# Kernel optimization log

Hardware: AMD Instinct MI355X
Metric: run time of the kernel (lower is better)

Reference implementation:

```python
import jax, jax.numpy as jnp
import numpy as np

B, N = 1, 512
C_S, C_Z, C_H, H, PQ, PV = 384, 128, 16, 12, 4, 8
INF, EPS = 1e5, 1e-8
HW_INIT = 0.541324854612918  # softplus^{-1}(1), ipa_point_weights_init_


def _rotary(t, rot_dim, theta=10000.0):
    # lucidrains interleaved rotary over residue axis (axis 1); rotates first rot_dim channels
    n = t.shape[1]
    inv_freq = 1.0 / (theta ** (jnp.arange(0, rot_dim, 2, dtype=jnp.float32) / rot_dim))
    freqs = jnp.arange(n, dtype=jnp.float32)[:, None] * inv_freq  # [N, rot_dim//2]
    cos = jnp.cos(freqs)[None, :, None, :].astype(t.dtype)
    sin = jnp.sin(freqs)[None, :, None, :].astype(t.dtype)
    tr, tp = t[..., :rot_dim], t[..., rot_dim:]
    x1, x2 = tr[..., 0::2], tr[..., 1::2]
    tr = jnp.stack([x1 * cos - x2 * sin, x1 * sin + x2 * cos], axis=-1).reshape(tr.shape)
    return jnp.concatenate([tr, tp], axis=-1)


def _ipa(s, z, rot, trans, mask, Wq, bq, Wkv, bkv, Wqp, bqp, Wkvp, bkvp, Wb, bb,
         head_weights, Whid, bhid, Wpair, bpair, Wpts, bpts, Wpn, bpn):
    Bx, Nx = s.shape[0], s.shape[1]
    q = (s @ Wq + bq).reshape(Bx, Nx, H, C_H)
    kv = (s @ Wkv + bkv).reshape(Bx, Nx, H, 2 * C_H)
    k, v = kv[..., :C_H], kv[..., C_H:]

    def make_pts(x, npts):
        # channel layout: [x-block, y-block, z-block] -> [B,N,H*npts,3], then rigid apply R@p+t
        x = jnp.stack(jnp.split(x, 3, axis=-1), axis=-1)
        x = jnp.einsum('bnij,bnpj->bnpi', rot, x) + trans[:, :, None, :]
        return x.reshape(Bx, Nx, H, npts, 3)

    q_pts = make_pts(s @ Wqp + bqp, PQ)
    kv_pts = make_pts(s @ Wkvp + bkvp, PQ + PV)
    k_pts, v_pts = kv_pts[..., :PQ, :], kv_pts[..., PQ:, :]

    q = _rotary(q, C_H // 2)
    k = _rotary(k, C_H // 2)

    a = jnp.einsum('bihc,bjhc->bhij', q, k) * np.sqrt(1.0 / (3 * C_H))
    a = a + np.sqrt(1.0 / 3.0) * (jnp.einsum('bijc,ch->bhij', z, Wb) + bb[None, :, None, None])
    d2 = jnp.sum((q_pts[:, :, None] - k_pts[:, None]) ** 2, axis=-1)  # [B,Ni,Nj,H,PQ]
    hw = jax.nn.softplus(head_weights) * np.sqrt(1.0 / (3 * (PQ * 9.0 / 2)))
    a = a + jnp.transpose(-0.5 * jnp.sum(d2 * hw[None, None, None, :, None], axis=-1), (0, 3, 1, 2))
    sq_mask = INF * (mask[:, :, None] * mask[:, None, :] - 1.0)
    a = jax.nn.softmax(a + sq_mask[:, None], axis=-1)  # [B,H,N,N]

    o = jnp.einsum('bhij,bjhc->bihc', a, v).reshape(Bx, Nx, H * C_H)
    o_pt = jnp.einsum('bhij,bjhpx->bihpx', a, v_pts)  # [B,N,H,PV,3]
    o_pt = jnp.einsum('bnji,bnhpj->bnhpi', rot, o_pt - trans[:, :, None, None, :])  # invert_apply
    o_pt_norm = jnp.sqrt(jnp.sum(o_pt ** 2, axis=-1) + EPS).reshape(Bx, Nx, H * PV)
    o_pt = o_pt.reshape(Bx, Nx, H * PV, 3)
    pts_feat = jnp.concatenate([o_pt[..., 0], o_pt[..., 1], o_pt[..., 2]], axis=-1)
    o_pair = jnp.einsum('bhij,bijc->bihc', a, z).reshape(Bx, Nx, H * C_Z)

    s_out = ((o @ Whid + bhid) + (o_pair @ Wpair + bpair)
             + (pts_feat @ Wpts + bpts) + (o_pt_norm @ Wpn + bpn))
    return s_out, a


def setup_inputs() -> dict:
    key = jax.random.key(0)
    ks = jax.random.split(key, 16)
    f = lambda i, shape: jax.random.normal(ks[i], shape, dtype=jnp.float32)
    sc = 0.02
    rot, _ = jnp.linalg.qr(f(2, (B, N, 3, 3)))
    return {
        's': f(0, (B, N, C_S)),
        'z': f(1, (B, N, N, C_Z)),
        'rot': rot,
        'trans': f(3, (B, N, 3)),
        'mask': jnp.ones((B, N), jnp.float32),
        'Wq': f(4, (C_S, H * C_H)) * sc, 'bq': jnp.zeros((H * C_H,), jnp.float32),
        'Wkv': f(5, (C_S, 2 * H * C_H)) * sc, 'bkv': jnp.zeros((2 * H * C_H,), jnp.float32),
        'Wqp': f(6, (C_S, H * PQ * 3)) * sc, 'bqp': jnp.zeros((H * PQ * 3,), jnp.float32),
        'Wkvp': f(7, (C_S, H * (PQ + PV) * 3)) * sc, 'bkvp': jnp.zeros((H * (PQ + PV) * 3,), jnp.float32),
        'Wb': f(8, (C_Z, H)) * sc, 'bb': jnp.zeros((H,), jnp.float32),
        'head_weights': jnp.full((H,), HW_INIT, jnp.float32),
        'Whid': f(9, (H * C_H, C_S)) * sc, 'bhid': jnp.zeros((C_S,), jnp.float32),
        'Wpair': f(10, (H * C_Z, C_S)) * sc, 'bpair': jnp.zeros((C_S,), jnp.float32),
        'Wpts': f(11, (H * PV * 3, C_S)) * sc, 'bpts': jnp.zeros((C_S,), jnp.float32),
        'Wpn': f(12, (H * PV, C_S)) * sc, 'bpn': jnp.zeros((C_S,), jnp.float32),
    }


def reference(s, z, rot, trans, mask, Wq, bq, Wkv, bkv, Wqp, bqp, Wkvp, bkvp, Wb, bb,
              head_weights, Whid, bhid, Wpair, bpair, Wpts, bpts, Wpn, bpn):
    return _ipa(s, z, rot, trans, mask, Wq, bq, Wkv, bkv, Wqp, bqp, Wkvp, bkvp, Wb, bb,
                head_weights, Whid, bhid, Wpair, bpair, Wpts, bpts, Wpn, bpn)
```

## Files before the change

kernel.cpp:

```cpp
#include <hip/hip_runtime.h>
#include <hip/hip_bf16.h>
#include <cmath>

#define N 512
#define C_S 384
#define C_Z 128
#define C_H 16
#define H 12
#define PQ 4
#define PV 8

#define NJC 4
#define JCHUNK (N / NJC)
#define NPART 2016
#define NFEAT 2112
#define NRAW 1152
#define KSPLIT 11
#define KCHUNK 192

#define WS_Q    0
#define WS_K    (WS_Q + N*H*C_H)
#define WS_V    (WS_K + N*H*C_H)
#define WS_QP   (WS_V + N*H*C_H)
#define WS_KP   (WS_QP + N*H*PQ*3)
#define WS_VP   (WS_KP + N*H*PQ*3)
#define WS_PART (WS_VP + N*H*PV*3)
#define WS_FEAT (WS_PART + N*NJC*NPART)
#define WS_RAW  WS_PART
#define WS_KT   (WS_PART + 1200000)
#define WS_KPT  (WS_KT + 98304)
#define WS_WBT  (WS_KPT + 73728)
#define WS_FOUT WS_PART

__global__ __launch_bounds__(256) void k_gemm_proj(
    const float* __restrict__ s,
    const float* __restrict__ Wq,  const float* __restrict__ bq,
    const float* __restrict__ Wkv, const float* __restrict__ bkv,
    const float* __restrict__ Wqp, const float* __restrict__ bqp,
    const float* __restrict__ Wkvp,const float* __restrict__ bkvp,
    float* __restrict__ raw_out)
{
    const int m0 = blockIdx.x * 64;
    const int c0 = blockIdx.y * 64;
    const int t  = threadIdx.x;
    const int tc = t & 15;
    const int tm = t >> 4;

    __shared__ float st[64 * 33];
    __shared__ float wt[32 * 64];

    float acc[4][4];
#pragma unroll
    for (int u = 0; u < 4; ++u) {
        int col = c0 + tc*4 + u;
        const float* b; int cb;
        if (col < 192)      { b = bq;   cb = 0; }
        else if (col < 576) { b = bkv;  cb = 192; }
        else if (col < 720) { b = bqp;  cb = 576; }
        else                { b = bkvp; cb = 720; }
        float bv = b[col - cb];
#pragma unroll
        for (int r = 0; r < 4; ++r) acc[r][u] = bv;
    }

    for (int k0 = 0; k0 < C_S; k0 += 32) {
        __syncthreads();
        for (int e = t; e < 512; e += 256) {
            int row = e >> 3, kq = e & 7;
            float4 v = *(const float4*)&s[(size_t)(m0 + row)*C_S + k0 + kq*4];
            st[row*33 + kq*4 + 0] = v.x;
            st[row*33 + kq*4 + 1] = v.y;
            st[row*33 + kq*4 + 2] = v.z;
            st[row*33 + kq*4 + 3] = v.w;
        }
        for (int e = t; e < 512; e += 256) {
            int kk = e >> 4, c4 = e & 15;
            int col = c0 + c4*4;
            const float* W; int ncol, cb;
            if (col < 192)      { W = Wq;   ncol = 192; cb = 0; }
            else if (col < 576) { W = Wkv;  ncol = 384; cb = 192; }
            else if (col < 720) { W = Wqp;  ncol = 144; cb = 576; }
            else                { W = Wkvp; ncol = 432; cb = 720; }
            float4 v = *(const float4*)&W[(size_t)(k0 + kk)*ncol + (col - cb)];
            *(float4*)&wt[kk*64 + c4*4] = v;
        }
        __syncthreads();

#pragma unroll 8
        for (int kk = 0; kk < 32; ++kk) {
            float4 w = *(const float4*)&wt[kk*64 + tc*4];
            float sv[4];
#pragma unroll
            for (int r = 0; r < 4; ++r) sv[r] = st[(tm*4 + r)*33 + kk];
#pragma unroll
            for (int r = 0; r < 4; ++r) {
                acc[r][0] += sv[r] * w.x;
                acc[r][1] += sv[r] * w.y;
                acc[r][2] += sv[r] * w.z;
                acc[r][3] += sv[r] * w.w;
            }
        }
    }

#pragma unroll
    for (int r = 0; r < 4; ++r) {
        float4 o = make_float4(acc[r][0], acc[r][1], acc[r][2], acc[r][3]);
        *(float4*)&raw_out[(size_t)(m0 + tm*4 + r)*NRAW + c0 + tc*4] = o;
    }
}

__global__ __launch_bounds__(256) void k_post(
    const float* __restrict__ raw_in, const float* __restrict__ rot,
    const float* __restrict__ trans, const float* __restrict__ Wb,
    float* __restrict__ ws)
{
    const int n = blockIdx.x;
    const int t = threadIdx.x;
    __shared__ float raw[NRAW];

    for (int idx = t; idx < NRAW; idx += 256) raw[idx] = raw_in[(size_t)n*NRAW + idx];
    __syncthreads();

    if (n == 0) {
        for (int idx = t; idx < H*C_Z; idx += 256) {
            int h = idx >> 7, c = idx & 127;
            ws[WS_WBT + h*128 + c] = Wb[c*H + h];
        }
    }

    float R[9], T[3];
#pragma unroll
    for (int u = 0; u < 9; ++u) R[u] = rot[n*9 + u];
#pragma unroll
    for (int u = 0; u < 3; ++u) T[u] = trans[n*3 + u];

    float* q    = ws + WS_Q;
    float* v    = ws + WS_V;
    float* qp   = ws + WS_QP;
    float* vp   = ws + WS_VP;
    float* kT4  = ws + WS_KT;
    float* kpT4 = ws + WS_KPT;

    for (int idx = t; idx < 1152; idx += 256) {
        if (idx < 192) {
            int h = idx >> 4, c = idx & 15;
            float val;
            if (c < 8) {
                int f = c >> 1;
                float x1 = raw[h*16 + 2*f];
                float x2 = raw[h*16 + 2*f + 1];
                float ang = (float)n * powf(10000.0f, -(float)(2*f) / 8.0f);
                float cs = cosf(ang), sn = sinf(ang);
                val = (c & 1) ? (x1*sn + x2*cs) : (x1*cs - x2*sn);
            } else {
                val = raw[h*16 + c];
            }
            q[n*192 + idx] = val;
        } else if (idx < 384) {
            int o = idx - 192, h = o >> 4, c = o & 15;
            float val;
            if (c < 8) {
                int f = c >> 1;
                float x1 = raw[192 + h*32 + 2*f];
                float x2 = raw[192 + h*32 + 2*f + 1];
                float ang = (float)n * powf(10000.0f, -(float)(2*f) / 8.0f);
                float cs = cosf(ang), sn = sinf(ang);
                val = (c & 1) ? (x1*sn + x2*cs) : (x1*cs - x2*sn);
            } else {
                val = raw[192 + h*32 + c];
            }
            kT4[((size_t)(o >> 2)*N + n)*4 + (o & 3)] = val;
        } else if (idx < 576) {
            int o = idx - 384, h = o >> 4, c = o & 15;
            v[n*192 + o] = raw[192 + h*32 + 16 + c];
        } else if (idx < 720) {
            int o = idx - 576;
            int hp = o / 3, ic = o - hp*3;
            float acc = T[ic];
#pragma unroll
            for (int j = 0; j < 3; ++j) acc += R[ic*3 + j] * raw[576 + j*48 + hp];
            qp[n*144 + o] = acc;
        } else {
            int o = idx - 720;
            int hp = o / 3, ic = o - hp*3;
            int h = hp / 12, p = hp - h*12;
            float acc = T[ic];
#pragma unroll
            for (int j = 0; j < 3; ++j) acc += R[ic*3 + j] * raw[720 + j*144 + hp];
            if (p < PQ) {
                int e = h*12 + p*3 + ic;
                kpT4[((size_t)(e >> 2)*N + n)*4 + (e & 3)] = acc;
            } else {
                vp[n*(H*PV*3) + (h*PV + (p - PQ))*3 + ic] = acc;
            }
        }
    }
}

__global__ __launch_bounds__(256) void k_logits(
    const float* __restrict__ ws, const float* __restrict__ z,
    const float* __restrict__ bb,
    const float* __restrict__ hwts, const float* __restrict__ mask,
    float* __restrict__ a_out)
{
    const int i  = blockIdx.x;
    const int j0 = blockIdx.y * 64;
    const int t  = threadIdx.x;
    const int j  = t & 63;
    const int jg = j0 + j;
    const int h0 = __builtin_amdgcn_readfirstlane(3 * (t >> 6));

    __shared__ float zt[64*132];

    float4 ra0, ra1, ra2, ra3, rb0, rb1, rb2, rb3;
    {
        const float* zbase = z + (((size_t)i*N) + j0)*C_Z;
        int e0 = t,       r0_ = e0 >> 4, c0_ = e0 & 15;
        int e1 = t + 256, r1_ = e1 >> 4, c1_ = e1 & 15;
        int e2 = t + 512, r2_ = e2 >> 4, c2_ = e2 & 15;
        int e3 = t + 768, r3_ = e3 >> 4, c3_ = e3 & 15;
        ra0 = *(const float4*)&zbase[(size_t)r0_*C_Z + c0_*4];
        ra1 = *(const float4*)&zbase[(size_t)r1_*C_Z + c1_*4];
        ra2 = *(const float4*)&zbase[(size_t)r2_*C_Z + c2_*4];
        ra3 = *(const float4*)&zbase[(size_t)r3_*C_Z + c3_*4];
        rb0 = *(const float4*)&zbase[(size_t)r0_*C_Z + 64 + c0_*4];
        rb1 = *(const float4*)&zbase[(size_t)r1_*C_Z + 64 + c1_*4];
        rb2 = *(const float4*)&zbase[(size_t)r2_*C_Z + 64 + c2_*4];
        rb3 = *(const float4*)&zbase[(size_t)r3_*C_Z + 64 + c3_*4];
    }

    const float* q    = ws + WS_Q  + (size_t)i*192;
    const float* qp   = ws + WS_QP + (size_t)i*144;
    const float* kT4  = ws + WS_KT;
    const float* kpT4 = ws + WS_KPT;

    const float c1 = sqrtf(1.0f / 48.0f);
    const float c2 = sqrtf(1.0f / 3.0f);
    const float mterm = 100000.0f * (mask[i] * mask[jg] - 1.0f);

    float qkd[3];
#pragma unroll
    for (int u = 0; u < 3; ++u) {
        const int h = h0 + u;
        float qk = 0.0f;
#pragma unroll
        for (int cq = 0; cq < 4; ++cq) {
            float4 kv = *(const float4*)&kT4[((size_t)(h*4 + cq)*N + jg)*4];
            qk += q[h*16 + cq*4 + 0]*kv.x + q[h*16 + cq*4 + 1]*kv.y
                + q[h*16 + cq*4 + 2]*kv.z + q[h*16 + cq*4 + 3]*kv.w;
        }
        float d2s = 0.0f;
#pragma unroll
        for (int eq = 0; eq < 3; ++eq) {
            float4 pv = *(const float4*)&kpT4[((size_t)(h*3 + eq)*N + jg)*4];
            float d;
            d = qp[h*12 + eq*4 + 0] - pv.x; d2s += d*d;
            d = qp[h*12 + eq*4 + 1] - pv.y; d2s += d*d;
            d = qp[h*12 + eq*4 + 2] - pv.z; d2s += d*d;
            d = qp[h*12 + eq*4 + 3] - pv.w; d2s += d*d;
        }
        float hw = log1pf(expf(hwts[h])) * sqrtf(1.0f / 54.0f);
        qkd[u] = c1*qk - 0.5f*hw*d2s + mterm + c2*bb[h];
    }

    {
        int e0 = t,       r0_ = e0 >> 4, c0_ = e0 & 15;
        int e1 = t + 256, r1_ = e1 >> 4, c1_ = e1 & 15;
        int e2 = t + 512, r2_ = e2 >> 4, c2_ = e2 & 15;
        int e3 = t + 768, r3_ = e3 >> 4, c3_ = e3 & 15;
        *(float4*)&zt[r0_*132 + c0_*4] = ra0;
        *(float4*)&zt[r1_*132 + c1_*4] = ra1;
        *(float4*)&zt[r2_*132 + c2_*4] = ra2;
        *(float4*)&zt[r3_*132 + c3_*4] = ra3;
    }
    __syncthreads();

    const float* w0 = ws + WS_WBT + (size_t)h0*128;
    float acc[3] = {0.0f, 0.0f, 0.0f};
#pragma unroll
    for (int c4 = 0; c4 < 16; ++c4) {
        float4 zv = *(const float4*)&zt[j*132 + c4*4];
        float4 b0 = *(const float4*)&w0[c4*4];
        float4 b1 = *(const float4*)&w0[128 + c4*4];
        float4 b2 = *(const float4*)&w0[256 + c4*4];
        acc[0] += zv.x*b0.x + zv.y*b0.y + zv.z*b0.z + zv.w*b0.w;
        acc[1] += zv.x*b1.x + zv.y*b1.y + zv.z*b1.z + zv.w*b1.w;
        acc[2] += zv.x*b2.x + zv.y*b2.y + zv.z*b2.z + zv.w*b2.w;
    }
    __syncthreads();

    {
        int e0 = t,       r0_ = e0 >> 4, c0_ = e0 & 15;
        int e1 = t + 256, r1_ = e1 >> 4, c1_ = e1 & 15;
        int e2 = t + 512, r2_ = e2 >> 4, c2_ = e2 & 15;
        int e3 = t + 768, r3_ = e3 >> 4, c3_ = e3 & 15;
        *(float4*)&zt[r0_*132 + 64 + c0_*4] = rb0;
        *(float4*)&zt[r1_*132 + 64 + c1_*4] = rb1;
        *(float4*)&zt[r2_*132 + 64 + c2_*4] = rb2;
        *(float4*)&zt[r3_*132 + 64 + c3_*4] = rb3;
    }
    __syncthreads();

#pragma unroll
    for (int c4 = 16; c4 < 32; ++c4) {
        float4 zv = *(const float4*)&zt[j*132 + c4*4];
        float4 b0 = *(const float4*)&w0[c4*4];
        float4 b1 = *(const float4*)&w0[128 + c4*4];
        float4 b2 = *(const float4*)&w0[256 + c4*4];
        acc[0] += zv.x*b0.x + zv.y*b0.y + zv.z*b0.z + zv.w*b0.w;
        acc[1] += zv.x*b1.x + zv.y*b1.y + zv.z*b1.z + zv.w*b1.w;
        acc[2] += zv.x*b2.x + zv.y*b2.y + zv.z*b2.z + zv.w*b2.w;
    }

#pragma unroll
    for (int u = 0; u < 3; ++u)
        a_out[((size_t)(h0 + u)*N + i)*N + jg] = qkd[u] + c2*acc[u];
}

__global__ __launch_bounds__(256) void k_softmax(float* __restrict__ a)
{
    const int row  = blockIdx.x*4 + (threadIdx.x >> 6);
    const int lane = threadIdx.x & 63;
    float* r = a + (size_t)row * N;

    float v[8];
    float m = -1e30f;
#pragma unroll
    for (int u = 0; u < 8; ++u) { v[u] = r[lane + 64*u]; m = fmaxf(m, v[u]); }
#pragma unroll
    for (int off = 32; off; off >>= 1) m = fmaxf(m, __shfl_xor(m, off));
    float ssum = 0.0f;
#pragma unroll
    for (int u = 0; u < 8; ++u) { v[u] = expf(v[u] - m); ssum += v[u]; }
#pragma unroll
    for (int off = 32; off; off >>= 1) ssum += __shfl_xor(ssum, off);
    float inv = 1.0f / ssum;
#pragma unroll
    for (int u = 0; u < 8; ++u) r[lane + 64*u] = v[u] * inv;
}

__global__ __launch_bounds__(256) void k_av(
    const float* __restrict__ a_full, const float* __restrict__ ws_ro,
    const float* __restrict__ z, float* __restrict__ ws)
{
    const int i  = blockIdx.x;
    const int jc = blockIdx.y;
    const int j0 = jc * JCHUNK;
    const int t  = threadIdx.x;

    __shared__ float a_s[H*JCHUNK];

    const float* v  = ws_ro + WS_V;
    const float* vp = ws_ro + WS_VP;
    float* part = ws + WS_PART + ((size_t)i*NJC + jc)*NPART;

    for (int e = t; e < H*JCHUNK; e += 256) {
        int h = e >> 7, jj = e & (JCHUNK-1);
        a_s[e] = a_full[((size_t)h*N + i)*N + j0 + jj];
    }
    __syncthreads();

    for (int idx = t; idx < 480; idx += 256) {
        float acc = 0.0f;
        if (idx < 192) {
            int h = idx >> 4;
            const float* vv = v + (size_t)j0*192 + idx;
            const float* ar = &a_s[h*JCHUNK];
#pragma unroll 8
            for (int jj = 0; jj < JCHUNK; ++jj) acc += ar[jj] * vv[(size_t)jj*192];
        } else {
            int o = idx - 192;
            int h = (o/3) >> 3;
            const float* vv = vp + (size_t)j0*288 + o;
            const float* ar = &a_s[h*JCHUNK];
#pragma unroll 8
            for (int jj = 0; jj < JCHUNK; ++jj) acc += ar[jj] * vv[(size_t)jj*288];
        }
        part[idx] = acc;
    }

    {
        const int c  = t & 127;
        const int hb = t >> 7;
        float acc[6];
#pragma unroll
        for (int u = 0; u < 6; ++u) acc[u] = 0.0f;
        const float* zi = z + ((size_t)i*N + j0)*C_Z + c;
        for (int jj = 0; jj < JCHUNK; jj += 8) {
            float zr[8];
#pragma unroll
            for (int r = 0; r < 8; ++r) zr[r] = zi[(size_t)(jj+r)*C_Z];
            float4 av0[6], av1[6];
#pragma unroll
            for (int u = 0; u < 6; ++u) {
                av0[u] = *(const float4*)&a_s[(hb + 2*u)*JCHUNK + jj];
                av1[u] = *(const float4*)&a_s[(hb + 2*u)*JCHUNK + jj + 4];
            }
#pragma unroll
            for (int u = 0; u < 6; ++u) {
                acc[u] += av0[u].x*zr[0] + av0[u].y*zr[1] + av0[u].z*zr[2] + av0[u].w*zr[3];
                acc[u] += av1[u].x*zr[4] + av1[u].y*zr[5] + av1[u].z*zr[6] + av1[u].w*zr[7];
            }
        }
#pragma unroll
        for (int u = 0; u < 6; ++u) part[480 + (hb + 2*u)*C_Z + c] = acc[u];
    }
}

__global__ __launch_bounds__(256) void k_feat(
    const float* __restrict__ rot, const float* __restrict__ trans,
    float* __restrict__ ws)
{
    const int i = blockIdx.x;
    const int t = threadIdx.x;

    __shared__ float vec[NPART];

    const float* part = ws + WS_PART + (size_t)i*NJC*NPART;
    float* feat = ws + WS_FEAT + (size_t)i*NFEAT;

    for (int e = t; e < NPART; e += 256) {
        float acc = 0.0f;
#pragma unroll
        for (int jc = 0; jc < NJC; ++jc) acc += part[(size_t)jc*NPART + e];
        vec[e] = acc;
    }
    __syncthreads();

    for (int e = t; e < NPART; e += 256) {
        if (e < 192)       feat[e] = vec[e];
        else if (e >= 480) feat[192 + (e - 480)] = vec[e];
    }

    if (t < H*PV) {
        const int hp = t;
        float T0 = trans[i*3+0], T1 = trans[i*3+1], T2 = trans[i*3+2];
        float px = vec[192 + hp*3 + 0] - T0;
        float py = vec[192 + hp*3 + 1] - T1;
        float pz = vec[192 + hp*3 + 2] - T2;
        const float* R = rot + i*9;
        float ox = R[0]*px + R[3]*py + R[6]*pz;
        float oy = R[1]*px + R[4]*py + R[7]*pz;
        float oz = R[2]*px + R[5]*py + R[8]*pz;
        feat[1728 + hp]       = ox;
        feat[1728 + 96 + hp]  = oy;
        feat[1728 + 192 + hp] = oz;
        feat[2016 + hp] = sqrtf(ox*ox + oy*oy + oz*oz + 1e-8f);
    }
}

__global__ __launch_bounds__(256) void k_final_part(
    const float* __restrict__ ws,
    const float* __restrict__ Whid, const float* __restrict__ Wpair,
    const float* __restrict__ Wpts, const float* __restrict__ Wpn,
    float* __restrict__ fout)
{
    const int m0 = blockIdx.x * 64;
    const int c0 = blockIdx.y * 64;
    const int kc = blockIdx.z;
    const int t  = threadIdx.x;
    const int tc = t & 15;
    const int tm = t >> 4;

    __shared__ float ft[64 * 33];
    __shared__ float wt[32 * 64];

    const float* feat = ws + WS_FEAT;

    float acc[4][4];
#pragma unroll
    for (int r = 0; r < 4; ++r)
#pragma unroll
        for (int u = 0; u < 4; ++u) acc[r][u] = 0.0f;

    const int kbase = kc * KCHUNK;
    for (int k0 = kbase; k0 < kbase + KCHUNK; k0 += 32) {
        const float* W; int r0;
        if (k0 < 192)       { W = Whid;  r0 = k0; }
        else if (k0 < 1728) { W = Wpair; r0 = k0 - 192; }
        else if (k0 < 2016) { W = Wpts;  r0 = k0 - 1728; }
        else                { W = Wpn;   r0 = k0 - 2016; }

        __syncthreads();
        for (int e = t; e < 512; e += 256) {
            int row = e >> 3, kq = e & 7;
            float4 v = *(const float4*)&feat[(size_t)(m0 + row)*NFEAT + k0 + kq*4];
            ft[row*33 + kq*4 + 0] = v.x;
            ft[row*33 + kq*4 + 1] = v.y;
            ft[row*33 + kq*4 + 2] = v.z;
            ft[row*33 + kq*4 + 3] = v.w;
        }
        for (int e = t; e < 512; e += 256) {
            int kk = e >> 4, c4 = e & 15;
            float4 v = *(const float4*)&W[(size_t)(r0 + kk)*C_S + c0 + c4*4];
            *(float4*)&wt[kk*64 + c4*4] = v;
        }
        __syncthreads();

#pragma unroll 8
        for (int kk = 0; kk < 32; ++kk) {
            float4 w = *(const float4*)&wt[kk*64 + tc*4];
            float sv[4];
#pragma unroll
            for (int r = 0; r < 4; ++r) sv[r] = ft[(tm*4 + r)*33 + kk];
#pragma unroll
            for (int r = 0; r < 4; ++r) {
                acc[r][0] += sv[r] * w.x;
                acc[r][1] += sv[r] * w.y;
                acc[r][2] += sv[r] * w.z;
                acc[r][3] += sv[r] * w.w;
            }
        }
    }

#pragma unroll
    for (int r = 0; r < 4; ++r) {
        float4 o = make_float4(acc[r][0], acc[r][1], acc[r][2], acc[r][3]);
        *(float4*)&fout[((size_t)kc*N + m0 + tm*4 + r)*C_S + c0 + tc*4] = o;
    }
}

__global__ __launch_bounds__(256) void k_red(
    const float* __restrict__ fout,
    const float* __restrict__ bhid, const float* __restrict__ bpair,
    const float* __restrict__ bpts, const float* __restrict__ bpn,
    float* __restrict__ s_out)
{
    const int idx = blockIdx.x * 256 + threadIdx.x;
    const int c = idx % C_S;
    float acc = bhid[c] + bpair[c] + bpts[c] + bpn[c];
#pragma unroll
    for (int kc = 0; kc < KSPLIT; ++kc)
        acc += fout[(size_t)kc*N*C_S + idx];
    s_out[idx] = acc;
}

extern "C" void kernel_launch(void* const* d_in, const int* in_sizes, int n_in,
                              void* d_out, int out_size, void* d_ws, size_t ws_size,
                              hipStream_t stream) {
    const float* s     = (const float*)d_in[0];
    const float* z     = (const float*)d_in[1];
    const float* rot   = (const float*)d_in[2];
    const float* trans = (const float*)d_in[3];
    const float* mask  = (const float*)d_in[4];
    const float* Wq    = (const float*)d_in[5];
    const float* bq    = (const float*)d_in[6];
    const float* Wkv   = (const float*)d_in[7];
    const float* bkv   = (const float*)d_in[8];
    const float* Wqp   = (const float*)d_in[9];
    const float* bqp   = (const float*)d_in[10];
    const float* Wkvp  = (const float*)d_in[11];
    const float* bkvp  = (const float*)d_in[12];
    const float* Wb    = (const float*)d_in[13];
    const float* bb    = (const float*)d_in[14];
    const float* hwts  = (const float*)d_in[15];
    const float* Whid  = (const float*)d_in[16];
    const float* bhid  = (const float*)d_in[17];
    const float* Wpair = (const float*)d_in[18];
    const float* bpair = (const float*)d_in[19];
    const float* Wpts  = (const float*)d_in[20];
    const float* bpts  = (const float*)d_in[21];
    const float* Wpn   = (const float*)d_in[22];
    const float* bpn   = (const float*)d_in[23];

    float* out   = (float*)d_out;
    float* s_out = out;
    float* a_out = out + N*C_S;
    float* ws    = (float*)d_ws;

    k_gemm_proj<<<dim3(8, 18), 256, 0, stream>>>(s, Wq, bq, Wkv, bkv, Wqp, bqp,
                                                 Wkvp, bkvp, ws + WS_RAW);
    k_post<<<N, 256, 0, stream>>>(ws + WS_RAW, rot, trans, Wb, ws);
    k_logits<<<dim3(N, 8), 256, 0, stream>>>(ws, z, bb, hwts, mask, a_out);
    k_softmax<<<(H*N)/4, 256, 0, stream>>>(a_out);
    k_av<<<dim3(N, NJC), 256, 0, stream>>>(a_out, ws, z, ws);
    k_feat<<<N, 256, 0, stream>>>(rot, trans, ws);
    k_final_part<<<dim3(8, 6, KSPLIT), 256, 0, stream>>>(ws, Whid, Wpair, Wpts,
                                                         Wpn, ws + WS_FOUT);
    k_red<<<(N*C_S)/256, 256, 0, stream>>>(ws + WS_FOUT, bhid, bpair, bpts, bpn,
                                           s_out);
}
```

Measured before the change: 161.0 us.

## Precompute z·Wb bias in separate kernel and fuse softmax into logits

A new kernel computes the pair-bias projection z·Wb for all heads up front, using cross-lane shuffle reductions, and writes it to workspace. The logits kernel now runs one block per query row, builds all 12 heads' logits in shared memory from that bias plus the qk and point terms, and applies the softmax in place. This removes the standalone softmax pass and its extra read and write of the attention matrix. In exchange it adds a write and read of a 12×N×N bias buffer, a shuffle-heavy reduction kernel, and a smaller grid for the logits kernel.

```diff
diff --git a/kernel.cpp b/kernel.cpp
--- a/kernel.cpp
+++ b/kernel.cpp
@@ -29,8 +29,53 @@
 #define WS_RAW  WS_PART
 #define WS_KT   (WS_PART + 1200000)
 #define WS_KPT  (WS_KT + 98304)
-#define WS_WBT  (WS_KPT + 73728)
+#define WS_ZB   (WS_KPT + 73728)
 #define WS_FOUT WS_PART
+
+__global__ __launch_bounds__(256) void k_zb(
+    const float* __restrict__ z, const float* __restrict__ Wb,
+    float* __restrict__ zb)
+{
+    const int i    = blockIdx.x;
+    const int half = blockIdx.y;
+    const int t    = threadIdx.x;
+    const int w    = t >> 6;
+    const int l    = t & 63;
+
+    float wbA[12], wbB[12];
+#pragma unroll
+    for (int h = 0; h < 12; ++h) {
+        wbA[h] = Wb[(2*l)*H + h];
+        wbB[h] = Wb[(2*l + 1)*H + h];
+    }
+
+    const int jbase = half*256 + w*64;
+    const float* zi = z + (size_t)i*N*C_Z;
+
+    for (int r = 0; r < 64; r += 2) {
+        const int j0 = jbase + r, j1 = jbase + r + 1;
+        float2 z0 = *(const float2*)&zi[(size_t)j0*C_Z + 2*l];
+        float2 z1 = *(const float2*)&zi[(size_t)j1*C_Z + 2*l];
+        float a0[12], a1[12];
+#pragma unroll
+        for (int h = 0; h < 12; ++h) {
+            a0[h] = z0.x*wbA[h] + z0.y*wbB[h];
+            a1[h] = z1.x*wbA[h] + z1.y*wbB[h];
+        }
+#pragma unroll
+        for (int h = 0; h < 12; ++h) {
+#pragma unroll
+            for (int off = 32; off; off >>= 1) {
+                a0[h] += __shfl_xor(a0[h], off);
+                a1[h] += __shfl_xor(a1[h], off);
+            }
+        }
+        if (l < 12) {
+            zb[(size_t)l*N*N + (size_t)i*N + j0] = a0[l];
+            zb[(size_t)l*N*N + (size_t)i*N + j1] = a1[l];
+        }
+    }
+}
 
 __global__ __launch_bounds__(256) void k_gemm_proj(
     const float* __restrict__ s,
@@ -111,8 +156,7 @@
 
 __global__ __launch_bounds__(256) void k_post(
     const float* __restrict__ raw_in, const float* __restrict__ rot,
-    const float* __restrict__ trans, const float* __restrict__ Wb,
-    float* __restrict__ ws)
+    const float* __restrict__ trans, float* __restrict__ ws)
 {
     const int n = blockIdx.x;
     const int t = threadIdx.x;
@@ -120,13 +164,6 @@
 
     for (int idx = t; idx < NRAW; idx += 256) raw[idx] = raw_in[(size_t)n*NRAW + idx];
     __syncthreads();
-
-    if (n == 0) {
-        for (int idx = t; idx < H*C_Z; idx += 256) {
-            int h = idx >> 7, c = idx & 127;
-            ws[WS_WBT + h*128 + c] = Wb[c*H + h];
-        }
-    }
 
     float R[9], T[3];
 #pragma unroll
@@ -197,37 +234,15 @@
     }
 }
 
-__global__ __launch_bounds__(256) void k_logits(
-    const float* __restrict__ ws, const float* __restrict__ z,
-    const float* __restrict__ bb,
-    const float* __restrict__ hwts, const float* __restrict__ mask,
-    float* __restrict__ a_out)
-{
-    const int i  = blockIdx.x;
-    const int j0 = blockIdx.y * 64;
-    const int t  = threadIdx.x;
-    const int j  = t & 63;
-    const int jg = j0 + j;
-    const int h0 = __builtin_amdgcn_readfirstlane(3 * (t >> 6));
-
-    __shared__ float zt[64*132];
-
-    float4 ra0, ra1, ra2, ra3, rb0, rb1, rb2, rb3;
-    {
-        const float* zbase = z + (((size_t)i*N) + j0)*C_Z;
-        int e0 = t,       r0_ = e0 >> 4, c0_ = e0 & 15;
-        int e1 = t + 256, r1_ = e1 >> 4, c1_ = e1 & 15;
-        int e2 = t + 512, r2_ = e2 >> 4, c2_ = e2 & 15;
-        int e3 = t + 768, r3_ = e3 >> 4, c3_ = e3 & 15;
-        ra0 = *(const float4*)&zbase[(size_t)r0_*C_Z + c0_*4];
-        ra1 = *(const float4*)&zbase[(size_t)r1_*C_Z + c1_*4];
-        ra2 = *(const float4*)&zbase[(size_t)r2_*C_Z + c2_*4];
-        ra3 = *(const float4*)&zbase[(size_t)r3_*C_Z + c3_*4];
-        rb0 = *(const float4*)&zbase[(size_t)r0_*C_Z + 64 + c0_*4];
-        rb1 = *(const float4*)&zbase[(size_t)r1_*C_Z + 64 + c1_*4];
-        rb2 = *(const float4*)&zbase[(size_t)r2_*C_Z + 64 + c2_*4];
-        rb3 = *(const float4*)&zbase[(size_t)r3_*C_Z + 64 + c3_*4];
-    }
+__global__ __launch_bounds__(256) void k_logits2(
+    const float* __restrict__ ws, const float* __restrict__ zb,
+    const float* __restrict__ bb, const float* __restrict__ hwts,
+    const float* __restrict__ mask, float* __restrict__ a_out)
+{
+    const int i = blockIdx.x;
+    const int t = threadIdx.x;
+
+    __shared__ float lg[H*N];
 
     const float* q    = ws + WS_Q  + (size_t)i*192;
     const float* qp   = ws + WS_QP + (size_t)i*144;
@@ -236,107 +251,56 @@
 
     const float c1 = sqrtf(1.0f / 48.0f);
     const float c2 = sqrtf(1.0f / 3.0f);
-    const float mterm = 100000.0f * (mask[i] * mask[jg] - 1.0f);
-
-    float qkd[3];
+    const float mi = mask[i];
+
+    for (int jt = 0; jt < 2; ++jt) {
+        const int j = jt*256 + t;
+        const float mterm = 100000.0f * (mi * mask[j] - 1.0f);
+        for (int h = 0; h < H; ++h) {
+            float qk = 0.0f;
+#pragma unroll
+            for (int cq = 0; cq < 4; ++cq) {
+                float4 kv = *(const float4*)&kT4[((size_t)(h*4 + cq)*N + j)*4];
+                qk += q[h*16 + cq*4 + 0]*kv.x + q[h*16 + cq*4 + 1]*kv.y
+                    + q[h*16 + cq*4 + 2]*kv.z + q[h*16 + cq*4 + 3]*kv.w;
+            }
+            float d2s = 0.0f;
+#pragma unroll
+            for (int eq = 0; eq < 3; ++eq) {
+                float4 pv = *(const float4*)&kpT4[((size_t)(h*3 + eq)*N + j)*4];
+                float d;
+                d = qp[h*12 + eq*4 + 0] - pv.x; d2s += d*d;
+                d = qp[h*12 + eq*4 + 1] - pv.y; d2s += d*d;
+                d = qp[h*12 + eq*4 + 2] - pv.z; d2s += d*d;
+                d = qp[h*12 + eq*4 + 3] - pv.w; d2s += d*d;
+            }
+            float hw = log1pf(expf(hwts[h])) * sqrtf(1.0f / 54.0f);
+            float zbv = zb[(size_t)h*N*N + (size_t)i*N + j];
+            lg[h*N + j] = c1*qk - 0.5f*hw*d2s + mterm + c2*(zbv + bb[h]);
+        }
+    }
+    __syncthreads();
+
+    const int w = t >> 6, lane = t & 63;
 #pragma unroll
     for (int u = 0; u < 3; ++u) {
-        const int h = h0 + u;
-        float qk = 0.0f;
-#pragma unroll
-        for (int cq = 0; cq < 4; ++cq) {
-            float4 kv = *(const float4*)&kT4[((size_t)(h*4 + cq)*N + jg)*4];
-            qk += q[h*16 + cq*4 + 0]*kv.x + q[h*16 + cq*4 + 1]*kv.y
-                + q[h*16 + cq*4 + 2]*kv.z + q[h*16 + cq*4 + 3]*kv.w;
-        }
-        float d2s = 0.0f;
-#pragma unroll
-        for (int eq = 0; eq < 3; ++eq) {
-            float4 pv = *(const float4*)&kpT4[((size_t)(h*3 + eq)*N + jg)*4];
-            float d;
-            d = qp[h*12 + eq*4 + 0] - pv.x; d2s += d*d;
-            d = qp[h*12 + eq*4 + 1] - pv.y; d2s += d*d;
-            d = qp[h*12 + eq*4 + 2] - pv.z; d2s += d*d;
-            d = qp[h*12 + eq*4 + 3] - pv.w; d2s += d*d;
-        }
-        float hw = log1pf(expf(hwts[h])) * sqrtf(1.0f / 54.0f);
-        qkd[u] = c1*qk - 0.5f*hw*d2s + mterm + c2*bb[h];
-    }
-
-    {
-        int e0 = t,       r0_ = e0 >> 4, c0_ = e0 & 15;
-        int e1 = t + 256, r1_ = e1 >> 4, c1_ = e1 & 15;
-        int e2 = t + 512, r2_ = e2 >> 4, c2_ = e2 & 15;
-        int e3 = t + 768, r3_ = e3 >> 4, c3_ = e3 & 15;
-        *(float4*)&zt[r0_*132 + c0_*4] = ra0;
-        *(float4*)&zt[r1_*132 + c1_*4] = ra1;
-        *(float4*)&zt[r2_*132 + c2_*4] = ra2;
-        *(float4*)&zt[r3_*132 + c3_*4] = ra3;
-    }
-    __syncthreads();
-
-    const float* w0 = ws + WS_WBT + (size_t)h0*128;
-    float acc[3] = {0.0f, 0.0f, 0.0f};
-#pragma unroll
-    for (int c4 = 0; c4 < 16; ++c4) {
-        float4 zv = *(const float4*)&zt[j*132 + c4*4];
-        float4 b0 = *(const float4*)&w0[c4*4];
-        float4 b1 = *(const float4*)&w0[128 + c4*4];
-        float4 b2 = *(const float4*)&w0[256 + c4*4];
-        acc[0] += zv.x*b0.x + zv.y*b0.y + zv.z*b0.z + zv.w*b0.w;
-        acc[1] += zv.x*b1.x + zv.y*b1.y + zv.z*b1.z + zv.w*b1.w;
-        acc[2] += zv.x*b2.x + zv.y*b2.y + zv.z*b2.z + zv.w*b2.w;
-    }
-    __syncthreads();
-
-    {
-        int e0 = t,       r0_ = e0 >> 4, c0_ = e0 & 15;
-        int e1 = t + 256, r1_ = e1 >> 4, c1_ = e1 & 15;
-        int e2 = t + 512, r2_ = e2 >> 4, c2_ = e2 & 15;
-        int e3 = t + 768, r3_ = e3 >> 4, c3_ = e3 & 15;
-        *(float4*)&zt[r0_*132 + 64 + c0_*4] = rb0;
-        *(float4*)&zt[r1_*132 + 64 + c1_*4] = rb1;
-        *(float4*)&zt[r2_*132 + 64 + c2_*4] = rb2;
-        *(float4*)&zt[r3_*132 + 64 + c3_*4] = rb3;
-    }
-    __syncthreads();
-
-#pragma unroll
-    for (int c4 = 16; c4 < 32; ++c4) {
-        float4 zv = *(const float4*)&zt[j*132 + c4*4];
-        float4 b0 = *(const float4*)&w0[c4*4];
-        float4 b1 = *(const float4*)&w0[128 + c4*4];
-        float4 b2 = *(const float4*)&w0[256 + c4*4];
-        acc[0] += zv.x*b0.x + zv.y*b0.y + zv.z*b0.z + zv.w*b0.w;
-        acc[1] += zv.x*b1.x + zv.y*b1.y + zv.z*b1.z + zv.w*b1.w;
-        acc[2] += zv.x*b2.x + zv.y*b2.y + zv.z*b2.z + zv.w*b2.w;
-    }
-
-#pragma unroll
-    for (int u = 0; u < 3; ++u)
-        a_out[((size_t)(h0 + u)*N + i)*N + jg] = qkd[u] + c2*acc[u];
-}
-
-__global__ __launch_bounds__(256) void k_softmax(float* __restrict__ a)
-{
-    const int row  = blockIdx.x*4 + (threadIdx.x >> 6);
-    const int lane = threadIdx.x & 63;
-    float* r = a + (size_t)row * N;
-
-    float v[8];
-    float m = -1e30f;
-#pragma unroll
-    for (int u = 0; u < 8; ++u) { v[u] = r[lane + 64*u]; m = fmaxf(m, v[u]); }
-#pragma unroll
-    for (int off = 32; off; off >>= 1) m = fmaxf(m, __shfl_xor(m, off));
-    float ssum = 0.0f;
-#pragma unroll
-    for (int u = 0; u < 8; ++u) { v[u] = expf(v[u] - m); ssum += v[u]; }
-#pragma unroll
-    for (int off = 32; off; off >>= 1) ssum += __shfl_xor(ssum, off);
-    float inv = 1.0f / ssum;
-#pragma unroll
-    for (int u = 0; u < 8; ++u) r[lane + 64*u] = v[u] * inv;
+        const int h = 3*w + u;
+        float v[8];
+        float m = -1e30f;
+#pragma unroll
+        for (int s = 0; s < 8; ++s) { v[s] = lg[h*N + lane + 64*s]; m = fmaxf(m, v[s]); }
+#pragma unroll
+        for (int off = 32; off; off >>= 1) m = fmaxf(m, __shfl_xor(m, off));
+        float ssum = 0.0f;
+#pragma unroll
+        for (int s = 0; s < 8; ++s) { v[s] = expf(v[s] - m); ssum += v[s]; }
+#pragma unroll
+        for (int off = 32; off; off >>= 1) ssum += __shfl_xor(ssum, off);
+        float inv = 1.0f / ssum;
+#pragma unroll
+        for (int s = 0; s < 8; ++s)
+            a_out[((size_t)h*N + i)*N + lane + 64*s] = v[s] * inv;
+    }
 }
 
 __global__ __launch_bounds__(256) void k_av(
@@ -568,11 +532,11 @@
     float* a_out = out + N*C_S;
     float* ws    = (float*)d_ws;
 
+    k_zb<<<dim3(N, 2), 256, 0, stream>>>(z, Wb, ws + WS_ZB);
     k_gemm_proj<<<dim3(8, 18), 256, 0, stream>>>(s, Wq, bq, Wkv, bkv, Wqp, bqp,
                                                  Wkvp, bkvp, ws + WS_RAW);
-    k_post<<<N, 256, 0, stream>>>(ws + WS_RAW, rot, trans, Wb, ws);
-    k_logits<<<dim3(N, 8), 256, 0, stream>>>(ws, z, bb, hwts, mask, a_out);
-    k_softmax<<<(H*N)/4, 256, 0, stream>>>(a_out);
+    k_post<<<N, 256, 0, stream>>>(ws + WS_RAW, rot, trans, ws);
+    k_logits2<<<N, 256, 0, stream>>>(ws, ws + WS_ZB, bb, hwts, mask, a_out);
     k_av<<<dim3(N, NJC), 256, 0, stream>>>(a_out, ws, z, ws);
     k_feat<<<N, 256, 0, stream>>>(rot, trans, ws);
     k_final_part<<<dim3(8, 6, KSPLIT), 256, 0, stream>>>(ws, Whid, Wpair, Wpts,
```

After: 340.9 us. 112% more time.

## Fuse softmax into logits and AV kernels via split max/sum statistics

Applied to the files above, without the earlier changes.

Removes the standalone softmax kernel. The logits kernel now computes a per-64-column max and exp-sum for each row segment and writes them to workspace reusing the K slot. The AV kernel merges these eight partials into a global max and inverse sum, normalises the logits as it loads them into shared memory, and writes the probabilities back to the attention output. This saves one full read-write pass over the 12x512x512 attention tensor and a launch, at the cost of extra shuffles and exps in logits. Separately, the rotary frequencies are replaced by precomputed constants instead of powf.

```diff
diff --git a/kernel.cpp b/kernel.cpp
--- a/kernel.cpp
+++ b/kernel.cpp
@@ -20,6 +20,7 @@
 
 #define WS_Q    0
 #define WS_K    (WS_Q + N*H*C_H)
+#define WS_SM   WS_K
 #define WS_V    (WS_K + N*H*C_H)
 #define WS_QP   (WS_V + N*H*C_H)
 #define WS_KP   (WS_QP + N*H*PQ*3)
@@ -147,9 +148,10 @@
             float val;
             if (c < 8) {
                 int f = c >> 1;
+                float fr = (f == 0) ? 1.0f : (f == 1) ? 0.1f : (f == 2) ? 0.01f : 0.001f;
+                float ang = (float)n * fr;
                 float x1 = raw[h*16 + 2*f];
                 float x2 = raw[h*16 + 2*f + 1];
-                float ang = (float)n * powf(10000.0f, -(float)(2*f) / 8.0f);
                 float cs = cosf(ang), sn = sinf(ang);
                 val = (c & 1) ? (x1*sn + x2*cs) : (x1*cs - x2*sn);
             } else {
@@ -161,9 +163,10 @@
             float val;
             if (c < 8) {
                 int f = c >> 1;
+                float fr = (f == 0) ? 1.0f : (f == 1) ? 0.1f : (f == 2) ? 0.01f : 0.001f;
+                float ang = (float)n * fr;
                 float x1 = raw[192 + h*32 + 2*f];
                 float x2 = raw[192 + h*32 + 2*f + 1];
-                float ang = (float)n * powf(10000.0f, -(float)(2*f) / 8.0f);
                 float cs = cosf(ang), sn = sinf(ang);
                 val = (c & 1) ? (x1*sn + x2*cs) : (x1*cs - x2*sn);
             } else {
@@ -198,7 +201,7 @@
 }
 
 __global__ __launch_bounds__(256) void k_logits(
-    const float* __restrict__ ws, const float* __restrict__ z,
+    float* __restrict__ ws, const float* __restrict__ z,
     const float* __restrict__ bb,
     const float* __restrict__ hwts, const float* __restrict__ mask,
     float* __restrict__ a_out)
@@ -312,35 +315,31 @@
         acc[2] += zv.x*b2.x + zv.y*b2.y + zv.z*b2.z + zv.w*b2.w;
     }
 
-#pragma unroll
-    for (int u = 0; u < 3; ++u)
-        a_out[((size_t)(h0 + u)*N + i)*N + jg] = qkd[u] + c2*acc[u];
-}
-
-__global__ __launch_bounds__(256) void k_softmax(float* __restrict__ a)
-{
-    const int row  = blockIdx.x*4 + (threadIdx.x >> 6);
-    const int lane = threadIdx.x & 63;
-    float* r = a + (size_t)row * N;
-
-    float v[8];
-    float m = -1e30f;
-#pragma unroll
-    for (int u = 0; u < 8; ++u) { v[u] = r[lane + 64*u]; m = fmaxf(m, v[u]); }
-#pragma unroll
-    for (int off = 32; off; off >>= 1) m = fmaxf(m, __shfl_xor(m, off));
-    float ssum = 0.0f;
-#pragma unroll
-    for (int u = 0; u < 8; ++u) { v[u] = expf(v[u] - m); ssum += v[u]; }
-#pragma unroll
-    for (int off = 32; off; off >>= 1) ssum += __shfl_xor(ssum, off);
-    float inv = 1.0f / ssum;
-#pragma unroll
-    for (int u = 0; u < 8; ++u) r[lane + 64*u] = v[u] * inv;
+    float lgv[3];
+#pragma unroll
+    for (int u = 0; u < 3; ++u) {
+        lgv[u] = qkd[u] + c2*acc[u];
+        a_out[((size_t)(h0 + u)*N + i)*N + jg] = lgv[u];
+    }
+
+    float* sm = ws + WS_SM;
+#pragma unroll
+    for (int u = 0; u < 3; ++u) {
+        float m = lgv[u];
+#pragma unroll
+        for (int off = 32; off; off >>= 1) m = fmaxf(m, __shfl_xor(m, off));
+        float sme = expf(lgv[u] - m);
+#pragma unroll
+        for (int off = 32; off; off >>= 1) sme += __shfl_xor(sme, off);
+        if (j == 0) {
+            sm[(size_t)i*192 + (h0 + u)*16 + blockIdx.y*2 + 0] = m;
+            sm[(size_t)i*192 + (h0 + u)*16 + blockIdx.y*2 + 1] = sme;
+        }
+    }
 }
 
 __global__ __launch_bounds__(256) void k_av(
-    const float* __restrict__ a_full, const float* __restrict__ ws_ro,
+    float* __restrict__ a_full, const float* __restrict__ ws_ro,
     const float* __restrict__ z, float* __restrict__ ws)
 {
     const int i  = blockIdx.x;
@@ -349,14 +348,32 @@
     const int t  = threadIdx.x;
 
     __shared__ float a_s[H*JCHUNK];
+    __shared__ float Msm[12], Ism[12];
 
     const float* v  = ws_ro + WS_V;
     const float* vp = ws_ro + WS_VP;
+    const float* sm = ws_ro + WS_SM;
     float* part = ws + WS_PART + ((size_t)i*NJC + jc)*NPART;
+
+    if (t < 12) {
+        const float* st = sm + (size_t)i*192 + t*16;
+        float M = -1e30f;
+#pragma unroll
+        for (int q8 = 0; q8 < 8; ++q8) M = fmaxf(M, st[q8*2]);
+        float S = 0.0f;
+#pragma unroll
+        for (int q8 = 0; q8 < 8; ++q8) S += st[q8*2 + 1] * expf(st[q8*2] - M);
+        Msm[t] = M;
+        Ism[t] = 1.0f / S;
+    }
+    __syncthreads();
 
     for (int e = t; e < H*JCHUNK; e += 256) {
         int h = e >> 7, jj = e & (JCHUNK-1);
-        a_s[e] = a_full[((size_t)h*N + i)*N + j0 + jj];
+        size_t gi = ((size_t)h*N + i)*N + j0 + jj;
+        float val = expf(a_full[gi] - Msm[h]) * Ism[h];
+        a_s[e] = val;
+        a_full[gi] = val;
     }
     __syncthreads();
 
@@ -572,7 +589,6 @@
                                                  Wkvp, bkvp, ws + WS_RAW);
     k_post<<<N, 256, 0, stream>>>(ws + WS_RAW, rot, trans, Wb, ws);
     k_logits<<<dim3(N, 8), 256, 0, stream>>>(ws, z, bb, hwts, mask, a_out);
-    k_softmax<<<(H*N)/4, 256, 0, stream>>>(a_out);
     k_av<<<dim3(N, NJC), 256, 0, stream>>>(a_out, ws, z, ws);
     k_feat<<<N, 256, 0, stream>>>(rot, trans, ws);
     k_final_part<<<dim3(8, 6, KSPLIT), 256, 0, stream>>>(ws, Whid, Wpair, Wpts,
```

Result: no change. 162.3 us (+0.8%).
